# Optimization experiments

Hardware: AMD Instinct MI355X
Metric: run time of the kernel (lower is better)

Reference implementation:

```python
import jax, jax.numpy as jnp
import numpy as np

H_GRID = 256
W_GRID = 256


def setup_inputs() -> dict:
    key = jax.random.key(0)
    k1, k2, k3, k4 = jax.random.split(key, 4)
    B, N = 8, 32768
    in_ch, out_ch = 14, 64
    xyzp = jax.random.uniform(k1, (B, N, 4), dtype=jnp.float32)  # x,y,t,p all in [0,1]
    features = jax.random.normal(k2, (B, N, in_ch), dtype=jnp.float32)
    W = jax.random.normal(k3, (9, in_ch + 2, out_ch), dtype=jnp.float32) * 0.05  # 3x3 kernel taps
    bias = jax.random.normal(k4, (out_ch,), dtype=jnp.float32) * 0.05
    return {"xyzp": xyzp, "features": features, "W": W, "bias": bias}


def reference(xyzp, features, W, bias):
    # SparseConv: voxelize points onto an (h+1)x(w+1) grid with 'mean' pooling of
    # duplicates, run a 3x3 submanifold sparse conv (inactive sites contribute 0),
    # then map results back to point order.
    h, w = H_GRID, W_GRID
    Hd, Wd = h + 1, w + 1  # round(y*h) in [0,h]
    B, N, _ = xyzp.shape
    Cin = features.shape[-1] + 2

    # yxb coordinates (note: column order [y, x] as in _get_yxb)
    y = jnp.clip(jnp.round(xyzp[..., 1] * h), 0, h).astype(jnp.int32).reshape(-1)
    x = jnp.clip(jnp.round(xyzp[..., 0] * w), 0, w).astype(jnp.int32).reshape(-1)
    b = jnp.repeat(jnp.arange(B, dtype=jnp.int32), N)

    # per-point features: [pos, neg, features]
    p = xyzp[..., 3:4]
    f = jnp.concatenate([p, 1.0 - p, features], axis=-1).reshape(B * N, Cin)

    # InputLayer mode='mean': scatter-mean duplicate coordinates into voxels
    flat = (b * Hd + y) * Wd + x  # [B*N]
    S = B * Hd * Wd
    vox_sum = jax.ops.segment_sum(f, flat, num_segments=S)            # [S, Cin]
    cnt = jax.ops.segment_sum(jnp.ones((B * N, 1), f.dtype), flat, num_segments=S)
    vox = vox_sum / jnp.maximum(cnt, 1.0)  # inactive voxels stay exactly 0

    # Submanifold 3x3 conv evaluated at each point's (active) site.
    offs = jnp.array([(dy, dx) for dy in (-1, 0, 1) for dx in (-1, 0, 1)], jnp.int32)  # [9,2]
    ny = y[:, None] + offs[None, :, 0]  # [B*N, 9]
    nx = x[:, None] + offs[None, :, 1]
    valid = (ny >= 0) & (ny < Hd) & (nx >= 0) & (nx < Wd)
    nidx = (b[:, None] * Hd + jnp.clip(ny, 0, Hd - 1)) * Wd + jnp.clip(nx, 0, Wd - 1)
    nb = vox[nidx] * valid[..., None].astype(f.dtype)  # [B*N, 9, Cin]; inactive -> 0

    out = jnp.einsum('pkc,kcd->pd', nb, W) + bias  # [B*N, out_ch]
    return out.reshape(B, N, -1)
```

## Files before the change

### kernel.cpp

```cpp
#include <hip/hip_runtime.h>

#define HD 257
#define WD 257
#define NB (8 * HD)
#define CAP 384
#define COUT 64
#define LROW 17
#define RPB 2
#define GPTS 64
#define BPTS 1024

typedef unsigned int uint;
typedef unsigned short ushort;
typedef short short8 __attribute__((ext_vector_type(8)));
typedef float f32x4 __attribute__((ext_vector_type(4)));

__device__ __forceinline__ uint pack_bf16(float a, float b) {
    uint ua = __float_as_uint(a), ub = __float_as_uint(b);
    ua += 0x7fffu + ((ua >> 16) & 1u);
    ub += 0x7fffu + ((ub >> 16) & 1u);
    return (ua >> 16) | (ub & 0xffff0000u);
}
__device__ __forceinline__ unsigned short bf16_1(float a) {
    uint ua = __float_as_uint(a);
    ua += 0x7fffu + ((ua >> 16) & 1u);
    return (unsigned short)(ua >> 16);
}

__global__ void zero_cnt_kernel(uint* __restrict__ cnt) {
    int i = blockIdx.x * blockDim.x + threadIdx.x;
    if (i < NB) cnt[i] = 0u;
}

__global__ __launch_bounds__(256) void bin_kernel(
    const float* __restrict__ xyzp,
    uint* __restrict__ cnt,
    ushort* __restrict__ pidx,
    int N) {
    __shared__ uint hist[HD];
    __shared__ uint base[HD];
    const int tid = threadIdx.x;
    const int b = blockIdx.y;
    const int p0 = blockIdx.x * BPTS;

    for (int i = tid; i < HD; i += 256) hist[i] = 0u;
    __syncthreads();

    const float4* xp = reinterpret_cast<const float4*>(xyzp) + (size_t)b * N;
    uint rec[BPTS / 256];
#pragma unroll
    for (int k = 0; k < BPTS / 256; ++k) {
        int i = p0 + tid + k * 256;
        float4 v = xp[i];
        int y = (int)fminf(fmaxf(rintf(v.y * 256.0f), 0.0f), 256.0f);
        uint r = atomicAdd(&hist[y], 1u);
        rec[k] = (uint)y | (r << 9);
    }
    __syncthreads();

    for (int y = tid; y < HD; y += 256) {
        uint h = hist[y];
        base[y] = h ? atomicAdd(&cnt[b * HD + y], h) : 0u;
    }
    __syncthreads();

#pragma unroll
    for (int k = 0; k < BPTS / 256; ++k) {
        int y = rec[k] & 511;
        uint slot = base[y] + (rec[k] >> 9);
        if (slot < CAP)
            pidx[(size_t)(b * HD + y) * CAP + slot] = (ushort)(p0 + tid + k * 256);
    }
}

__global__ __launch_bounds__(256) void accum_kernel(
    const uint* __restrict__ cnt,
    const ushort* __restrict__ pidx,
    const float* __restrict__ xyzp,
    const float* __restrict__ feat,
    uint* __restrict__ voxn,
    int logN) {
    __shared__ float l[RPB * WD * LROW];
    const int tid = threadIdx.x;
    const int bucket0 = blockIdx.x * RPB;
    for (int i = tid; i < RPB * WD * LROW; i += 256) l[i] = 0.0f;
    __syncthreads();

    uint n0 = min(cnt[bucket0], (uint)CAP);
    uint n1 = min(cnt[bucket0 + 1], (uint)CAP);
    uint ntot = n0 + n1;
    for (uint s = tid; s < ntot; s += 256) {
        int r = (s >= n0) ? 1 : 0;
        uint slot = s - (r ? n0 : 0u);
        int bucket = bucket0 + r;
        int b = bucket / HD;
        uint lp = pidx[(size_t)bucket * CAP + slot];
        int p = (b << logN) + (int)lp;
        float4 v = reinterpret_cast<const float4*>(xyzp)[p];
        int x = (int)fminf(fmaxf(rintf(v.x * 256.0f), 0.0f), 256.0f);
        float* cell = l + (r * WD + x) * LROW;
        atomicAdd(&cell[0], v.w);
        atomicAdd(&cell[1], 1.0f - v.w);
        const float2* f2 = reinterpret_cast<const float2*>(feat + (size_t)p * 14);
#pragma unroll
        for (int j = 0; j < 7; ++j) {
            float2 fv = f2[j];
            atomicAdd(&cell[2 + 2 * j], fv.x);
            atomicAdd(&cell[3 + 2 * j], fv.y);
        }
    }
    __syncthreads();

    for (int i = tid; i < RPB * WD; i += 256) {
        int r = i / WD;
        int x = i - r * WD;
        const float* c = l + (r * WD + x) * LROW;
        float inv = __builtin_amdgcn_rcpf(fmaxf(c[0] + c[1], 1.0f));
        uint o[8];
#pragma unroll
        for (int j = 0; j < 8; ++j)
            o[j] = pack_bf16(c[2 * j] * inv, c[2 * j + 1] * inv);
        uint4* op = reinterpret_cast<uint4*>(voxn + ((size_t)(bucket0 + r) * WD + x) * 8);
        op[0] = make_uint4(o[0], o[1], o[2], o[3]);
        op[1] = make_uint4(o[4], o[5], o[6], o[7]);
    }
}

__global__ __launch_bounds__(256) void gather_mfma_kernel(
    const float* __restrict__ xyzp,
    const uint* __restrict__ voxn,
    const float* __restrict__ W,
    const float* __restrict__ bias,
    float* __restrict__ out, int logN) {
    __shared__ __align__(16) char sA[GPTS * 336];
    __shared__ int sCell[GPTS];
    __shared__ uint sYX[GPTS];

    const int tid = threadIdx.x;
    const int lane = tid & 63;
    const int w = tid >> 6;
    const int p0 = blockIdx.x * GPTS;
    const int hi = lane >> 4;
    const int lo = lane & 15;

    if (tid < GPTS) {
        float4 v = reinterpret_cast<const float4*>(xyzp)[p0 + tid];
        int y = (int)fminf(fmaxf(rintf(v.y * 256.0f), 0.0f), 256.0f);
        int x = (int)fminf(fmaxf(rintf(v.x * 256.0f), 0.0f), 256.0f);
        int b = (p0 + tid) >> logN;
        sCell[tid] = (b * HD + y) * WD + x;
        sYX[tid] = ((uint)y << 16) | (uint)x;
    }

    short8 bfrag[5];
    float bv = bias[w * 16 + lo];
#pragma unroll
    for (int s = 0; s < 5; ++s) {
        int kbase = s * 32 + hi * 8;
        short8 f;
#pragma unroll
        for (int j = 0; j < 8; ++j) {
            int k = kbase + j;
            float wv = (k < 144) ? W[(size_t)k * 64 + w * 16 + lo] : 0.0f;
            f[j] = (short)bf16_1(wv);
        }
        bfrag[s] = f;
    }
    __syncthreads();

    for (int idx = tid; idx < GPTS * 18; idx += 256) {
        int i = idx / 18;
        int r = idx - i * 18;
        int seg = r / 6;
        int h = r - seg * 6;
        int kx = h >> 1;
        int half = h & 1;
        uint yx = sYX[i];
        int y = (int)(yx >> 16), x = (int)(yx & 0xffffu);
        int ny = y + seg - 1, nx = x + kx - 1;
        uint4 val = make_uint4(0, 0, 0, 0);
        if ((uint)ny <= 256u && (uint)nx <= 256u) {
            size_t ncell = (size_t)sCell[i] + (size_t)((seg - 1) * WD + (kx - 1));
            val = *reinterpret_cast<const uint4*>(
                reinterpret_cast<const char*>(voxn) + ncell * 32 + (size_t)half * 16);
        }
        *reinterpret_cast<uint4*>(sA + i * 336 + (seg * 3 + kx) * 32 + half * 16) = val;
    }
    if (tid < GPTS * 2) {
        int i = tid >> 1, h = tid & 1;
        *reinterpret_cast<uint4*>(sA + i * 336 + 288 + h * 16) = make_uint4(0, 0, 0, 0);
    }
    __syncthreads();

    f32x4 acc[4];
#pragma unroll
    for (int mt = 0; mt < 4; ++mt) acc[mt] = (f32x4){bv, bv, bv, bv};

#pragma unroll
    for (int mt = 0; mt < 4; ++mt) {
        const char* abase = sA + (mt * 16 + lo) * 336 + hi * 16;
#pragma unroll
        for (int s = 0; s < 5; ++s) {
            short8 a = *reinterpret_cast<const short8*>(abase + s * 64);
            acc[mt] = __builtin_amdgcn_mfma_f32_16x16x32_bf16(a, bfrag[s], acc[mt], 0, 0, 0);
        }
    }

#pragma unroll
    for (int mt = 0; mt < 4; ++mt)
#pragma unroll
        for (int r = 0; r < 4; ++r) {
            int row = mt * 16 + hi * 4 + r;
            out[(size_t)(p0 + row) * 64 + w * 16 + lo] = acc[mt][r];
        }
}

extern "C" void kernel_launch(void* const* d_in, const int* in_sizes, int n_in,
                              void* d_out, int out_size, void* d_ws, size_t ws_size,
                              hipStream_t stream) {
    const float* xyzp = (const float*)d_in[0];
    const float* feat = (const float*)d_in[1];
    const float* W    = (const float*)d_in[2];
    const float* bias = (const float*)d_in[3];
    float* out = (float*)d_out;

    const int BN = in_sizes[0] / 4;
    const int B = 8;
    const int N = BN / B;
    int logN = 0;
    while ((1 << logN) < N) ++logN;

    uint* cnt = (uint*)d_ws;
    ushort* pidx = (ushort*)(cnt + NB);
    uint* voxn = (uint*)(pidx + (size_t)NB * CAP);
    (void)ws_size;

    zero_cnt_kernel<<<(NB + 255) / 256, 256, 0, stream>>>(cnt);
    dim3 bgrid(N / BPTS, B);
    bin_kernel<<<bgrid, 256, 0, stream>>>(xyzp, cnt, pidx, N);
    accum_kernel<<<NB / RPB, 256, 0, stream>>>(cnt, pidx, xyzp, feat, voxn, logN);
    gather_mfma_kernel<<<BN / GPTS, 256, 0, stream>>>(xyzp, voxn, W, bias, out, logN);
}
```

Measured before the change: 74.02 us.

## Replace global atomic row bins with per-chunk slots and pre-pack bf16 weights

Binning now writes per-chunk row counts and point indices into fixed per-(row,chunk) slots, with no global atomics. This removes the zero-count kernel and the cross-block atomicAdd. The accumulate kernel finds each slot with a linear prefix scan over 64 chunk counts held in shared memory, which adds per-thread search work. A small new kernel converts W to bf16 MFMA fragments once, so each gather block loads packed uint4 values instead of converting 40 floats itself. Capping each chunk at 32 points per row could drop points if a chunk ever holds more than 32 in one row.

Result: slower. 79.35 us (+7.2%).

```diff
diff --git a/kernel.cpp b/kernel.cpp
--- a/kernel.cpp
+++ b/kernel.cpp
@@ -3,12 +3,13 @@
 #define HD 257
 #define WD 257
 #define NB (8 * HD)
-#define CAP 384
+#define NCHUNK 32
+#define CAPC 32
+#define BPTS 1024
 #define COUT 64
 #define LROW 17
 #define RPB 2
 #define GPTS 64
-#define BPTS 1024
 
 typedef unsigned int uint;
 typedef unsigned short ushort;
@@ -21,28 +22,34 @@
     ub += 0x7fffu + ((ub >> 16) & 1u);
     return (ua >> 16) | (ub & 0xffff0000u);
 }
-__device__ __forceinline__ unsigned short bf16_1(float a) {
-    uint ua = __float_as_uint(a);
-    ua += 0x7fffu + ((ua >> 16) & 1u);
-    return (unsigned short)(ua >> 16);
-}
-
-__global__ void zero_cnt_kernel(uint* __restrict__ cnt) {
-    int i = blockIdx.x * blockDim.x + threadIdx.x;
-    if (i < NB) cnt[i] = 0u;
+
+__global__ void wprep_kernel(const float* __restrict__ W, uint4* __restrict__ Wb) {
+    int idx = blockIdx.x * blockDim.x + threadIdx.x;
+    if (idx >= 5 * 4 * 64) return;
+    int s = idx >> 8;
+    int hi = (idx >> 6) & 3;
+    int col = idx & 63;
+    uint o[4];
+#pragma unroll
+    for (int jj = 0; jj < 4; ++jj) {
+        int k0 = s * 32 + hi * 8 + 2 * jj;
+        float fl = (k0 < 144) ? W[(size_t)k0 * 64 + col] : 0.0f;
+        float fh = (k0 + 1 < 144) ? W[(size_t)(k0 + 1) * 64 + col] : 0.0f;
+        o[jj] = pack_bf16(fl, fh);
+    }
+    Wb[idx] = make_uint4(o[0], o[1], o[2], o[3]);
 }
 
 __global__ __launch_bounds__(256) void bin_kernel(
     const float* __restrict__ xyzp,
-    uint* __restrict__ cnt,
+    uint* __restrict__ cnt2,
     ushort* __restrict__ pidx,
     int N) {
     __shared__ uint hist[HD];
-    __shared__ uint base[HD];
     const int tid = threadIdx.x;
+    const int chunk = blockIdx.x;
     const int b = blockIdx.y;
-    const int p0 = blockIdx.x * BPTS;
-
+    const int p0 = chunk * BPTS;
     for (int i = tid; i < HD; i += 256) hist[i] = 0u;
     __syncthreads();
 
@@ -58,43 +65,50 @@
     }
     __syncthreads();
 
-    for (int y = tid; y < HD; y += 256) {
-        uint h = hist[y];
-        base[y] = h ? atomicAdd(&cnt[b * HD + y], h) : 0u;
-    }
-    __syncthreads();
+    for (int y = tid; y < HD; y += 256)
+        cnt2[(size_t)(b * HD + y) * NCHUNK + chunk] = min(hist[y], (uint)CAPC);
 
 #pragma unroll
     for (int k = 0; k < BPTS / 256; ++k) {
         int y = rec[k] & 511;
-        uint slot = base[y] + (rec[k] >> 9);
-        if (slot < CAP)
-            pidx[(size_t)(b * HD + y) * CAP + slot] = (ushort)(p0 + tid + k * 256);
+        uint r = rec[k] >> 9;
+        if (r < CAPC)
+            pidx[((size_t)(b * HD + y) * NCHUNK + chunk) * CAPC + r] =
+                (ushort)(p0 + tid + k * 256);
     }
 }
 
 __global__ __launch_bounds__(256) void accum_kernel(
-    const uint* __restrict__ cnt,
+    const uint* __restrict__ cnt2,
     const ushort* __restrict__ pidx,
     const float* __restrict__ xyzp,
     const float* __restrict__ feat,
     uint* __restrict__ voxn,
     int logN) {
     __shared__ float l[RPB * WD * LROW];
+    __shared__ uint pc[RPB * NCHUNK];
     const int tid = threadIdx.x;
     const int bucket0 = blockIdx.x * RPB;
     for (int i = tid; i < RPB * WD * LROW; i += 256) l[i] = 0.0f;
-    __syncthreads();
-
-    uint n0 = min(cnt[bucket0], (uint)CAP);
-    uint n1 = min(cnt[bucket0 + 1], (uint)CAP);
-    uint ntot = n0 + n1;
-    for (uint s = tid; s < ntot; s += 256) {
-        int r = (s >= n0) ? 1 : 0;
-        uint slot = s - (r ? n0 : 0u);
+    if (tid < RPB * NCHUNK)
+        pc[tid] = cnt2[(size_t)bucket0 * NCHUNK + tid];
+    __syncthreads();
+
+    for (uint s = tid; ; s += 256) {
+        uint c = 0, acc = 0;
+        while (c < RPB * NCHUNK) {
+            uint h = pc[c];
+            if (s < acc + h) break;
+            acc += h;
+            ++c;
+        }
+        if (c == RPB * NCHUNK) break;
+        uint j = s - acc;
+        int r = (int)(c >> 5);
+        int chunk = (int)(c & 31);
         int bucket = bucket0 + r;
         int b = bucket / HD;
-        uint lp = pidx[(size_t)bucket * CAP + slot];
+        uint lp = pidx[((size_t)bucket * NCHUNK + chunk) * CAPC + j];
         int p = (b << logN) + (int)lp;
         float4 v = reinterpret_cast<const float4*>(xyzp)[p];
         int x = (int)fminf(fmaxf(rintf(v.x * 256.0f), 0.0f), 256.0f);
@@ -103,10 +117,10 @@
         atomicAdd(&cell[1], 1.0f - v.w);
         const float2* f2 = reinterpret_cast<const float2*>(feat + (size_t)p * 14);
 #pragma unroll
-        for (int j = 0; j < 7; ++j) {
-            float2 fv = f2[j];
-            atomicAdd(&cell[2 + 2 * j], fv.x);
-            atomicAdd(&cell[3 + 2 * j], fv.y);
+        for (int jj = 0; jj < 7; ++jj) {
+            float2 fv = f2[jj];
+            atomicAdd(&cell[2 + 2 * jj], fv.x);
+            atomicAdd(&cell[3 + 2 * jj], fv.y);
         }
     }
     __syncthreads();
@@ -129,7 +143,7 @@
 __global__ __launch_bounds__(256) void gather_mfma_kernel(
     const float* __restrict__ xyzp,
     const uint* __restrict__ voxn,
-    const float* __restrict__ W,
+    const uint4* __restrict__ Wb,
     const float* __restrict__ bias,
     float* __restrict__ out, int logN) {
     __shared__ __align__(16) char sA[GPTS * 336];
@@ -154,17 +168,11 @@
 
     short8 bfrag[5];
     float bv = bias[w * 16 + lo];
-#pragma unroll
-    for (int s = 0; s < 5; ++s) {
-        int kbase = s * 32 + hi * 8;
-        short8 f;
-#pragma unroll
-        for (int j = 0; j < 8; ++j) {
-            int k = kbase + j;
-            float wv = (k < 144) ? W[(size_t)k * 64 + w * 16 + lo] : 0.0f;
-            f[j] = (short)bf16_1(wv);
-        }
-        bfrag[s] = f;
+    {
+        const uint4* wb = Wb + hi * 64 + (w * 16 + lo);
+#pragma unroll
+        for (int s = 0; s < 5; ++s)
+            bfrag[s] = *reinterpret_cast<const short8*>(&wb[(size_t)s * 256]);
     }
     __syncthreads();
 
@@ -230,14 +238,15 @@
     int logN = 0;
     while ((1 << logN) < N) ++logN;
 
-    uint* cnt = (uint*)d_ws;
-    ushort* pidx = (ushort*)(cnt + NB);
-    uint* voxn = (uint*)(pidx + (size_t)NB * CAP);
+    uint4* Wb = (uint4*)d_ws;
+    uint* cnt2 = (uint*)((char*)d_ws + 5 * 4 * 64 * 16);
+    ushort* pidx = (ushort*)((char*)cnt2 + (size_t)NB * NCHUNK * 4);
+    uint* voxn = (uint*)((char*)pidx + (size_t)NB * NCHUNK * CAPC * 2);
     (void)ws_size;
 
-    zero_cnt_kernel<<<(NB + 255) / 256, 256, 0, stream>>>(cnt);
-    dim3 bgrid(N / BPTS, B);
-    bin_kernel<<<bgrid, 256, 0, stream>>>(xyzp, cnt, pidx, N);
-    accum_kernel<<<NB / RPB, 256, 0, stream>>>(cnt, pidx, xyzp, feat, voxn, logN);
-    gather_mfma_kernel<<<BN / GPTS, 256, 0, stream>>>(xyzp, voxn, W, bias, out, logN);
-}
+    wprep_kernel<<<5, 256, 0, stream>>>(W, Wb);
+    dim3 bgrid(NCHUNK, B);
+    bin_kernel<<<bgrid, 256, 0, stream>>>(xyzp, cnt2, pidx, N);
+    accum_kernel<<<NB / RPB, 256, 0, stream>>>(cnt2, pidx, xyzp, feat, voxn, logN);
+    gather_mfma_kernel<<<BN / GPTS, 256, 0, stream>>>(xyzp, voxn, Wb, bias, out, logN);
+}
```
